# Kernel tuning notes

Hardware: AMD Instinct MI355X
Metric: run time of the kernel (lower is better)

Reference implementation:

```python
import jax, jax.numpy as jnp
import numpy as np

B, T, F, H = 16, 512, 32, 128
EPS = 1e-5


def _layer_norm(y, g, b):
    mu = jnp.mean(y, axis=-1, keepdims=True)
    var = jnp.mean(jnp.square(y - mu), axis=-1, keepdims=True)
    return (y - mu) * jax.lax.rsqrt(var + EPS) * g + b


def setup_inputs() -> dict:
    key = jax.random.key(0)
    ks = jax.random.split(key, 16)
    s = 0.1  # small param scale
    return {
        "x": jax.random.normal(ks[0], (B, T, F), jnp.float32),
        # weight GRN (input_size == hidden == F, skip is Identity)
        "wg_fc1_w": jax.random.normal(ks[1], (F, F), jnp.float32) * s,
        "wg_fc1_b": jnp.zeros((F,), jnp.float32),
        "wg_fc2_w": jax.random.normal(ks[2], (2 * F, F), jnp.float32) * s,
        "wg_fc2_b": jnp.zeros((2 * F,), jnp.float32),
        "wg_ln_g": jnp.ones((F,), jnp.float32),
        "wg_ln_b": jnp.zeros((F,), jnp.float32),
        # per-feature GRNs (input_size=1 -> hidden H), batched over F
        "f_fc1_w": jax.random.normal(ks[3], (F, H), jnp.float32) * s,   # torch Linear(1,H).weight squeezed
        "f_fc1_b": jax.random.normal(ks[4], (F, H), jnp.float32) * s,
        "f_fc2_w": jax.random.normal(ks[5], (F, 2 * H, H), jnp.float32) * s,
        "f_fc2_b": jax.random.normal(ks[6], (F, 2 * H), jnp.float32) * s,
        "f_skip_w": jax.random.normal(ks[7], (F, H), jnp.float32) * s,  # Linear(1,H).weight squeezed
        "f_skip_b": jax.random.normal(ks[8], (F, H), jnp.float32) * s,
        "f_ln_g": jnp.ones((F, H), jnp.float32),
        "f_ln_b": jnp.zeros((F, H), jnp.float32),
    }


def reference(x, wg_fc1_w, wg_fc1_b, wg_fc2_w, wg_fc2_b, wg_ln_g, wg_ln_b,
              f_fc1_w, f_fc1_b, f_fc2_w, f_fc2_b, f_skip_w, f_skip_b,
              f_ln_g, f_ln_b):
    # --- weight GRN over the feature axis: [B,T,F] -> [B,T,F] ---
    h = jax.nn.elu(jnp.einsum('btf,gf->btg', x, wg_fc1_w) + wg_fc1_b)
    h2 = jnp.einsum('btg,kg->btk', h, wg_fc2_w) + wg_fc2_b  # [B,T,2F]
    a, g = jnp.split(h2, 2, axis=-1)
    glu = a * jax.nn.sigmoid(g)
    weights = jax.nn.softmax(_layer_norm(x + glu, wg_ln_g, wg_ln_b), axis=-1)  # [B,T,F]

    # --- all F per-feature GRNs batched (input width 1) ---
    xe = x[..., None]                                   # [B,T,F,1]
    h = jax.nn.elu(xe * f_fc1_w + f_fc1_b)              # [B,T,F,H]
    h2 = jnp.einsum('btfh,fgh->btfg', h, f_fc2_w) + f_fc2_b  # [B,T,F,2H]
    a, g = jnp.split(h2, 2, axis=-1)
    glu = a * jax.nn.sigmoid(g)                         # [B,T,F,H]
    res = xe * f_skip_w + f_skip_b                      # [B,T,F,H]
    y = _layer_norm(res + glu, f_ln_g, f_ln_b)          # per-feature LN params [F,H]

    # --- softmax-weighted combine ---
    return jnp.einsum('btf,btfh->bth', weights, y)      # [B,T,H]
```

## Files before the change

kernel.cpp:

```cpp
#include <hip/hip_runtime.h>
#include <cstdint>
#include <cstddef>

#define EPS 1e-5f

typedef float    f4    __attribute__((ext_vector_type(4)));
typedef _Float16 half8 __attribute__((ext_vector_type(8)));

#define S_XS 33
#define LOG2E 1.44269504088896f

__device__ __forceinline__ float fexp(float x)  { return __builtin_amdgcn_exp2f(x * LOG2E); }
__device__ __forceinline__ float frcp(float x)  { return __builtin_amdgcn_rcpf(x); }
__device__ __forceinline__ float frsq(float x)  { return __builtin_amdgcn_rsqf(x); }
__device__ __forceinline__ float fsig(float g)  { return frcp(1.f + __builtin_amdgcn_exp2f(g * -LOG2E)); }
__device__ __forceinline__ float felu(float t)  { return t > 0.f ? t : fexp(t) - 1.f; }

__global__ __launch_bounds__(256) void k_prep(
    const float* __restrict__ in_w2, _Float16* __restrict__ w2c,
    const float* __restrict__ x, const float* __restrict__ w1,
    const float* __restrict__ b1, const float* __restrict__ w2,
    const float* __restrict__ b2, const float* __restrict__ lng,
    const float* __restrict__ lnb,
    float* __restrict__ x_t, float* __restrict__ wts_t,
    float* __restrict__ outp)
{
    __shared__ float w1s[32 * S_XS];
    __shared__ float w2s[64 * S_XS];
    __shared__ float xsW[32 * S_XS];
    __shared__ float ytile[32 * S_XS];

    const int bid = blockIdx.x;
    const int tid = threadIdx.x;

    if (bid < 512) {
        int t = bid * 256 + tid;
        int q  = t & 3;
        int g  = (t >> 2) & 255;
        int fk = t >> 10;
        int f = fk >> 2, kq = fk & 3;
        const float* ip = in_w2 + ((size_t)f * 256 + g) * 128 + kq * 32 + q * 8;
        f4 v0 = *(const f4*)ip, v1 = *(const f4*)(ip + 4);
        half8 h;
        #pragma unroll
        for (int i = 0; i < 4; ++i) { h[i] = (_Float16)v0[i]; h[4 + i] = (_Float16)v1[i]; }
        *(half8*)(w2c + (size_t)fk * 8192 + q * 2048 + g * 8) = h;
        return;
    }

    if (bid >= 768) {
        int t = (bid - 768) * 256 + tid;
        f4 z; z[0] = 0.f; z[1] = 0.f; z[2] = 0.f; z[3] = 0.f;
        for (int i = t; i < 262144; i += 4096)
            *(f4*)(outp + (size_t)i * 4) = z;
        return;
    }

    const int lane = tid & 63;
    const int f = lane & 31;
    const int wv = tid >> 6;
    const int row0 = (bid - 512) * 32;

    for (int i = tid; i < 1024; i += 256) {
        int r = i >> 5, c = i & 31;
        w1s[r * S_XS + c] = w1[i];
        xsW[r * S_XS + c] = x[(size_t)row0 * 32 + i];
    }
    for (int i = tid; i < 2048; i += 256) {
        int r = i >> 5, c = i & 31;
        w2s[r * S_XS + c] = w2[i];
    }
    const float b1f = b1[f], b2a = b2[f], b2g = b2[f + 32];
    const float lgf = lng[f], lbf = lnb[f];
    __syncthreads();

    for (int rr = 0; rr < 8; ++rr) {
        const int r = wv * 8 + rr;
        float acc = b1f;
        #pragma unroll
        for (int k = 0; k < 32; ++k)
            acc = fmaf(w1s[f * S_XS + k], xsW[r * S_XS + k], acc);
        float hval = felu(acc);

        float a = b2a, g = b2g;
        #pragma unroll
        for (int k = 0; k < 32; ++k) {
            float hk = __shfl(hval, k, 64);
            a = fmaf(w2s[f * S_XS + k], hk, a);
            g = fmaf(w2s[(f + 32) * S_XS + k], hk, g);
        }
        float xv = xsW[r * S_XS + f];
        float v = xv + a * fsig(g);

        float s = v;
        #pragma unroll
        for (int o = 1; o < 64; o <<= 1) s += __shfl_xor(s, o, 64);
        float mu = s * (1.f / 64.f);
        float d = v - mu;
        float sq = d * d;
        #pragma unroll
        for (int o = 1; o < 64; o <<= 1) sq += __shfl_xor(sq, o, 64);
        float y = d * frsq(sq * (1.f / 64.f) + EPS) * lgf + lbf;

        float m = y;
        #pragma unroll
        for (int o = 1; o < 64; o <<= 1) m = fmaxf(m, __shfl_xor(m, o, 64));
        float e = fexp(y - m);
        float se = e;
        #pragma unroll
        for (int o = 1; o < 64; o <<= 1) se += __shfl_xor(se, o, 64);
        if (lane < 32) ytile[r * S_XS + f] = e * 2.f * frcp(se);
    }
    __syncthreads();
    for (int i = tid; i < 1024; i += 256) {
        int ff = i >> 5, r = i & 31;
        x_t[(size_t)ff * 8192 + row0 + r]   = xsW[r * S_XS + ff];
        wts_t[(size_t)ff * 8192 + row0 + r] = ytile[r * S_XS + ff];
    }
}

__global__ __launch_bounds__(256, 3) void k_main(
    const _Float16* __restrict__ w2c,
    const float* __restrict__ x_t,
    const float* __restrict__ wts_t,
    const float* __restrict__ fc1w, const float* __restrict__ fc1b,
    const float* __restrict__ fc2b,
    const float* __restrict__ skw, const float* __restrict__ skb,
    const float* __restrict__ lng, const float* __restrict__ lnb,
    float* __restrict__ out)
{
    __shared__ float red[2][2][4][4][2][2];

    const int tid = threadIdx.x;
    const int fbase = (blockIdx.x >> 7) * 4;
    const int row0 = (blockIdx.x & 127) * 64;

    const int lane = tid & 63;
    const int wv = tid >> 6;
    const int rowhalf = wv >> 1;
    const int hhalf = wv & 1;
    const int l15 = lane & 15;
    const int q = lane >> 4;

    float out_acc[2][4][4];
    #pragma unroll
    for (int g2 = 0; g2 < 2; ++g2)
        #pragma unroll
        for (int nt = 0; nt < 4; ++nt)
            #pragma unroll
            for (int rg = 0; rg < 4; ++rg) out_acc[g2][nt][rg] = 0.f;

    for (int fi = 0; fi < 4; ++fi) {
        const int f = fbase + fi;
        const float* xcol = x_t + (size_t)f * 8192 + row0 + rowhalf * 32;
        const float* wcol = wts_t + (size_t)f * 8192 + row0 + rowhalf * 32;
        const float xv0 = xcol[l15];
        const float xv1 = xcol[16 + l15];

        half8 A0[4], A1[4];
        #pragma unroll
        for (int kq = 0; kq < 4; ++kq) {
            const float* wp = fc1w + f * 128 + kq * 32 + 8 * q;
            const float* bp = fc1b + f * 128 + kq * 32 + 8 * q;
            f4 w0 = *(const f4*)wp, w1v = *(const f4*)(wp + 4);
            f4 b0 = *(const f4*)bp, b1v = *(const f4*)(bp + 4);
            #pragma unroll
            for (int j = 0; j < 4; ++j) {
                A0[kq][j]     = (_Float16)felu(fmaf(xv0, w0[j], b0[j]));
                A0[kq][4 + j] = (_Float16)felu(fmaf(xv0, w1v[j], b1v[j]));
                A1[kq][j]     = (_Float16)felu(fmaf(xv1, w0[j], b0[j]));
                A1[kq][4 + j] = (_Float16)felu(fmaf(xv1, w1v[j], b1v[j]));
            }
        }

        f4 accA0[4], accG0[4], accA1[4], accG1[4];
        #pragma unroll
        for (int nt = 0; nt < 4; ++nt) {
            const int h = hhalf * 64 + nt * 16 + l15;
            float ba = fc2b[f * 256 + h];
            float bg = fc2b[f * 256 + 128 + h];
            #pragma unroll
            for (int rg = 0; rg < 4; ++rg) {
                accA0[nt][rg] = ba; accA1[nt][rg] = ba;
                accG0[nt][rg] = bg; accG1[nt][rg] = bg;
            }
        }

        const _Float16* bp0 = w2c + (size_t)f * 4 * 8192
                            + q * 2048 + hhalf * 512 + l15 * 8;

        #pragma unroll
        for (int kq = 0; kq < 4; ++kq) {
            const _Float16* bp = bp0 + kq * 8192;
            half8 B0 = *(const half8*)(bp);
            half8 B1 = *(const half8*)(bp + 128);
            half8 B2 = *(const half8*)(bp + 256);
            half8 B3 = *(const half8*)(bp + 384);
            accA0[0] = __builtin_amdgcn_mfma_f32_16x16x32_f16(A0[kq], B0, accA0[0], 0, 0, 0);
            accA1[0] = __builtin_amdgcn_mfma_f32_16x16x32_f16(A1[kq], B0, accA1[0], 0, 0, 0);
            accA0[1] = __builtin_amdgcn_mfma_f32_16x16x32_f16(A0[kq], B1, accA0[1], 0, 0, 0);
            accA1[1] = __builtin_amdgcn_mfma_f32_16x16x32_f16(A1[kq], B1, accA1[1], 0, 0, 0);
            accA0[2] = __builtin_amdgcn_mfma_f32_16x16x32_f16(A0[kq], B2, accA0[2], 0, 0, 0);
            accA1[2] = __builtin_amdgcn_mfma_f32_16x16x32_f16(A1[kq], B2, accA1[2], 0, 0, 0);
            accA0[3] = __builtin_amdgcn_mfma_f32_16x16x32_f16(A0[kq], B3, accA0[3], 0, 0, 0);
            accA1[3] = __builtin_amdgcn_mfma_f32_16x16x32_f16(A1[kq], B3, accA1[3], 0, 0, 0);
            half8 G0 = *(const half8*)(bp + 1024);
            half8 G1 = *(const half8*)(bp + 1152);
            half8 G2 = *(const half8*)(bp + 1280);
            half8 G3 = *(const half8*)(bp + 1408);
            accG0[0] = __builtin_amdgcn_mfma_f32_16x16x32_f16(A0[kq], G0, accG0[0], 0, 0, 0);
            accG1[0] = __builtin_amdgcn_mfma_f32_16x16x32_f16(A1[kq], G0, accG1[0], 0, 0, 0);
            accG0[1] = __builtin_amdgcn_mfma_f32_16x16x32_f16(A0[kq], G1, accG0[1], 0, 0, 0);
            accG1[1] = __builtin_amdgcn_mfma_f32_16x16x32_f16(A1[kq], G1, accG1[1], 0, 0, 0);
            accG0[2] = __builtin_amdgcn_mfma_f32_16x16x32_f16(A0[kq], G2, accG0[2], 0, 0, 0);
            accG1[2] = __builtin_amdgcn_mfma_f32_16x16x32_f16(A1[kq], G2, accG1[2], 0, 0, 0);
            accG0[3] = __builtin_amdgcn_mfma_f32_16x16x32_f16(A0[kq], G3, accG0[3], 0, 0, 0);
            accG1[3] = __builtin_amdgcn_mfma_f32_16x16x32_f16(A1[kq], G3, accG1[3], 0, 0, 0);
        }

        float s0[4], sq0[4], s1[4], sq1[4];
        #pragma unroll
        for (int rg = 0; rg < 4; ++rg) { s0[rg] = 0.f; sq0[rg] = 0.f; s1[rg] = 0.f; sq1[rg] = 0.f; }

        f4 xr0 = *(const f4*)(xcol + 4 * q);
        f4 xr1 = *(const f4*)(xcol + 16 + 4 * q);
        #pragma unroll
        for (int nt = 0; nt < 4; ++nt) {
            const int h = hhalf * 64 + nt * 16 + l15;
            float sw = skw[f * 128 + h];
            float sb = skb[f * 128 + h];
            #pragma unroll
            for (int rg = 0; rg < 4; ++rg) {
                float v0 = fmaf(xr0[rg], sw, sb) + accA0[nt][rg] * fsig(accG0[nt][rg]);
                float v1 = fmaf(xr1[rg], sw, sb) + accA1[nt][rg] * fsig(accG1[nt][rg]);
                accA0[nt][rg] = v0;
                accA1[nt][rg] = v1;
                s0[rg] += v0; sq0[rg] = fmaf(v0, v0, sq0[rg]);
                s1[rg] += v1; sq1[rg] = fmaf(v1, v1, sq1[rg]);
            }
        }
        #pragma unroll
        for (int o = 1; o < 16; o <<= 1) {
            #pragma unroll
            for (int rg = 0; rg < 4; ++rg) {
                s0[rg] += __shfl_xor(s0[rg], o, 64);
                sq0[rg] += __shfl_xor(sq0[rg], o, 64);
                s1[rg] += __shfl_xor(s1[rg], o, 64);
                sq1[rg] += __shfl_xor(sq1[rg], o, 64);
            }
        }
        if (l15 == 0) {
            #pragma unroll
            for (int rg = 0; rg < 4; ++rg) {
                red[rowhalf][0][q][rg][hhalf][0] = s0[rg];
                red[rowhalf][0][q][rg][hhalf][1] = sq0[rg];
                red[rowhalf][1][q][rg][hhalf][0] = s1[rg];
                red[rowhalf][1][q][rg][hhalf][1] = sq1[rg];
            }
        }
        __syncthreads();

        f4 wr0 = *(const f4*)(wcol + 4 * q);
        f4 wr1 = *(const f4*)(wcol + 16 + 4 * q);
        float mu0[4], c10[4], mu1[4], c11[4];
        #pragma unroll
        for (int rg = 0; rg < 4; ++rg) {
            float st0 = s0[rg] + red[rowhalf][0][q][rg][hhalf ^ 1][0];
            float qt0 = sq0[rg] + red[rowhalf][0][q][rg][hhalf ^ 1][1];
            float st1 = s1[rg] + red[rowhalf][1][q][rg][hhalf ^ 1][0];
            float qt1 = sq1[rg] + red[rowhalf][1][q][rg][hhalf ^ 1][1];
            mu0[rg] = st0 * (1.f / 128.f);
            mu1[rg] = st1 * (1.f / 128.f);
            float var0 = qt0 * (1.f / 128.f) - mu0[rg] * mu0[rg];
            float var1 = qt1 * (1.f / 128.f) - mu1[rg] * mu1[rg];
            c10[rg] = wr0[rg] * frsq(fmaxf(var0, 0.f) + EPS);
            c11[rg] = wr1[rg] * frsq(fmaxf(var1, 0.f) + EPS);
        }
        #pragma unroll
        for (int nt = 0; nt < 4; ++nt) {
            const int h = hhalf * 64 + nt * 16 + l15;
            float lg = lng[f * 128 + h];
            float lb = lnb[f * 128 + h];
            #pragma unroll
            for (int rg = 0; rg < 4; ++rg) {
                float u0 = (accA0[nt][rg] - mu0[rg]) * c10[rg];
                float u1 = (accA1[nt][rg] - mu1[rg]) * c11[rg];
                out_acc[0][nt][rg] = fmaf(u0, lg, fmaf(wr0[rg], lb, out_acc[0][nt][rg]));
                out_acc[1][nt][rg] = fmaf(u1, lg, fmaf(wr1[rg], lb, out_acc[1][nt][rg]));
            }
        }
        __syncthreads();
    }

    #pragma unroll
    for (int g2 = 0; g2 < 2; ++g2) {
        #pragma unroll
        for (int nt = 0; nt < 4; ++nt) {
            #pragma unroll
            for (int rg = 0; rg < 4; ++rg) {
                const int r = row0 + rowhalf * 32 + g2 * 16 + 4 * q + rg;
                atomicAdd(&out[(size_t)r * 128 + hhalf * 64 + nt * 16 + l15],
                          out_acc[g2][nt][rg]);
            }
        }
    }
}

extern "C" void kernel_launch(void* const* d_in, const int* in_sizes, int n_in,
                              void* d_out, int out_size, void* d_ws, size_t ws_size,
                              hipStream_t stream) {
    const float* x     = (const float*)d_in[0];
    const float* wg1w  = (const float*)d_in[1];
    const float* wg1b  = (const float*)d_in[2];
    const float* wg2w  = (const float*)d_in[3];
    const float* wg2b  = (const float*)d_in[4];
    const float* wglng = (const float*)d_in[5];
    const float* wglnb = (const float*)d_in[6];
    const float* fc1w  = (const float*)d_in[7];
    const float* fc1b  = (const float*)d_in[8];
    const float* fc2w  = (const float*)d_in[9];
    const float* fc2b  = (const float*)d_in[10];
    const float* skw   = (const float*)d_in[11];
    const float* skb   = (const float*)d_in[12];
    const float* lng   = (const float*)d_in[13];
    const float* lnb   = (const float*)d_in[14];
    float* out = (float*)d_out;

    char* ws = (char*)d_ws;
    _Float16* w2c = (_Float16*)ws;
    float* x_t    = (float*)(ws + (2u << 20));
    float* wts_t  = (float*)(ws + (3u << 20));

    k_prep<<<dim3(784), dim3(256), 0, stream>>>(fc2w, w2c, x, wg1w, wg1b,
                                                wg2w, wg2b, wglng, wglnb,
                                                x_t, wts_t, out);
    k_main<<<dim3(1024), dim3(256), 0, stream>>>(w2c, x_t, wts_t, fc1w, fc1b,
                                                 fc2b, skw, skb, lng, lnb, out);
}
```

Measured before the change: 179.2 us.

## Stage fc2 weight chunks into LDS with double-buffered async global loads

The per-feature fc2 weight chunks are now copied from global memory straight into a double-buffered LDS array using global_load_lds. The next chunk is prefetched while MFMAs consume the current one. The four waves of a block share one copy in LDS instead of each wave fetching its B/G fragments from global/L2, which removes the duplicate loads between the two row-half waves. In exchange the kernel uses 32 KB more LDS per block and a block-wide barrier after every k-chunk, which can add stalls and may limit occupancy.

```diff
diff --git a/kernel.cpp b/kernel.cpp
--- a/kernel.cpp
+++ b/kernel.cpp
@@ -9,6 +9,11 @@
 
 #define S_XS 33
 #define LOG2E 1.44269504088896f
+
+#define GLD_LDS16(gp, lp)                                        \
+    __builtin_amdgcn_global_load_lds(                            \
+        (const __attribute__((address_space(1))) void*)(gp),     \
+        (__attribute__((address_space(3))) void*)(lp), 16, 0, 0)
 
 __device__ __forceinline__ float fexp(float x)  { return __builtin_amdgcn_exp2f(x * LOG2E); }
 __device__ __forceinline__ float frcp(float x)  { return __builtin_amdgcn_rcpf(x); }
@@ -129,6 +134,7 @@
     const float* __restrict__ lng, const float* __restrict__ lnb,
     float* __restrict__ out)
 {
+    __shared__ __align__(16) _Float16 bchunk[2][8192];
     __shared__ float red[2][2][4][4][2][2];
 
     const int tid = threadIdx.x;
@@ -141,6 +147,15 @@
     const int hhalf = wv & 1;
     const int l15 = lane & 15;
     const int q = lane >> 4;
+    const int boff = q * 2048 + hhalf * 512 + l15 * 8;
+
+    auto stage = [&](int c) {
+        const _Float16* gp = w2c + ((size_t)(fbase + (c >> 2)) * 4 + (c & 3)) * 8192;
+        #pragma unroll
+        for (int r = 0; r < 4; ++r)
+            GLD_LDS16(gp + (r * 256 + tid) * 8,
+                      &bchunk[c & 1][(r * 256 + tid) * 8]);
+    };
 
     float out_acc[2][4][4];
     #pragma unroll
@@ -150,6 +165,10 @@
             #pragma unroll
             for (int rg = 0; rg < 4; ++rg) out_acc[g2][nt][rg] = 0.f;
 
+    stage(0);
+    __syncthreads();
+
+    int c = 0;
     for (int fi = 0; fi < 4; ++fi) {
         const int f = fbase + fi;
         const float* xcol = x_t + (size_t)f * 8192 + row0 + rowhalf * 32;
@@ -186,36 +205,20 @@
             }
         }
 
-        const _Float16* bp0 = w2c + (size_t)f * 4 * 8192
-                            + q * 2048 + hhalf * 512 + l15 * 8;
-
-        #pragma unroll
-        for (int kq = 0; kq < 4; ++kq) {
-            const _Float16* bp = bp0 + kq * 8192;
-            half8 B0 = *(const half8*)(bp);
-            half8 B1 = *(const half8*)(bp + 128);
-            half8 B2 = *(const half8*)(bp + 256);
-            half8 B3 = *(const half8*)(bp + 384);
-            accA0[0] = __builtin_amdgcn_mfma_f32_16x16x32_f16(A0[kq], B0, accA0[0], 0, 0, 0);
-            accA1[0] = __builtin_amdgcn_mfma_f32_16x16x32_f16(A1[kq], B0, accA1[0], 0, 0, 0);
-            accA0[1] = __builtin_amdgcn_mfma_f32_16x16x32_f16(A0[kq], B1, accA0[1], 0, 0, 0);
-            accA1[1] = __builtin_amdgcn_mfma_f32_16x16x32_f16(A1[kq], B1, accA1[1], 0, 0, 0);
-            accA0[2] = __builtin_amdgcn_mfma_f32_16x16x32_f16(A0[kq], B2, accA0[2], 0, 0, 0);
-            accA1[2] = __builtin_amdgcn_mfma_f32_16x16x32_f16(A1[kq], B2, accA1[2], 0, 0, 0);
-            accA0[3] = __builtin_amdgcn_mfma_f32_16x16x32_f16(A0[kq], B3, accA0[3], 0, 0, 0);
-            accA1[3] = __builtin_amdgcn_mfma_f32_16x16x32_f16(A1[kq], B3, accA1[3], 0, 0, 0);
-            half8 G0 = *(const half8*)(bp + 1024);
-            half8 G1 = *(const half8*)(bp + 1152);
-            half8 G2 = *(const half8*)(bp + 1280);
-            half8 G3 = *(const half8*)(bp + 1408);
-            accG0[0] = __builtin_amdgcn_mfma_f32_16x16x32_f16(A0[kq], G0, accG0[0], 0, 0, 0);
-            accG1[0] = __builtin_amdgcn_mfma_f32_16x16x32_f16(A1[kq], G0, accG1[0], 0, 0, 0);
-            accG0[1] = __builtin_amdgcn_mfma_f32_16x16x32_f16(A0[kq], G1, accG0[1], 0, 0, 0);
-            accG1[1] = __builtin_amdgcn_mfma_f32_16x16x32_f16(A1[kq], G1, accG1[1], 0, 0, 0);
-            accG0[2] = __builtin_amdgcn_mfma_f32_16x16x32_f16(A0[kq], G2, accG0[2], 0, 0, 0);
-            accG1[2] = __builtin_amdgcn_mfma_f32_16x16x32_f16(A1[kq], G2, accG1[2], 0, 0, 0);
-            accG0[3] = __builtin_amdgcn_mfma_f32_16x16x32_f16(A0[kq], G3, accG0[3], 0, 0, 0);
-            accG1[3] = __builtin_amdgcn_mfma_f32_16x16x32_f16(A1[kq], G3, accG1[3], 0, 0, 0);
+        #pragma unroll
+        for (int kq = 0; kq < 4; ++kq, ++c) {
+            if (c + 1 < 16) stage(c + 1);
+            const _Float16* bb = &bchunk[c & 1][boff];
+            #pragma unroll
+            for (int nt = 0; nt < 4; ++nt) {
+                half8 B = *(const half8*)(bb + nt * 128);
+                accA0[nt] = __builtin_amdgcn_mfma_f32_16x16x32_f16(A0[kq], B, accA0[nt], 0, 0, 0);
+                accA1[nt] = __builtin_amdgcn_mfma_f32_16x16x32_f16(A1[kq], B, accA1[nt], 0, 0, 0);
+                half8 G = *(const half8*)(bb + 1024 + nt * 128);
+                accG0[nt] = __builtin_amdgcn_mfma_f32_16x16x32_f16(A0[kq], G, accG0[nt], 0, 0, 0);
+                accG1[nt] = __builtin_amdgcn_mfma_f32_16x16x32_f16(A1[kq], G, accG1[nt], 0, 0, 0);
+            }
+            __syncthreads();
         }
 
         float s0[4], sq0[4], s1[4], sq1[4];
```

Result: faster. 175.4 us (-2.1%).
